# Performance work log

Measured on AMD Instinct MI355X. Metric: run time of the kernel, lower is better.

## Reference

```python
import jax, jax.numpy as jnp
import numpy as np

B, D, L, H = 256, 512, 64, 300


def setup_inputs() -> dict:
    key = jax.random.key(0)
    ks = jax.random.split(key, 16)
    s = 0.05  # weight init scale to keep activations sane through ReLU chains
    return {
        "x": jax.random.normal(ks[0], (B, D), jnp.float32),
        "eps": jax.random.normal(ks[1], (B, L), jnp.float32),
        "W": jax.random.normal(ks[2], (D, L), jnp.float32) * s,
        "enc1_w": jax.random.normal(ks[3], (H, D), jnp.float32) * s,
        "enc1_b": jax.random.normal(ks[4], (H,), jnp.float32) * s,
        "enc2_w": jax.random.normal(ks[5], (H, H), jnp.float32) * s,
        "enc2_b": jax.random.normal(ks[6], (H,), jnp.float32) * s,
        "zm_w": jax.random.normal(ks[7], (L, H), jnp.float32) * s,
        "zm_b": jax.random.normal(ks[8], (L,), jnp.float32) * s,
        "zv_w": jax.random.normal(ks[9], (L, H), jnp.float32) * s,
        "zv_b": jax.random.normal(ks[10], (L,), jnp.float32) * s,
        "gen1_w": jax.random.normal(ks[11], (H, L), jnp.float32) * s,
        "gen2_w": jax.random.normal(ks[12], (H, H), jnp.float32) * s,
        "gen2_b": jax.random.normal(ks[13], (H,), jnp.float32) * s,
        "head_w": jax.random.normal(ks[14], (D, H), jnp.float32) * s,
        "head_b": jax.random.normal(ks[15], (D,), jnp.float32) * s,
    }


def reference(x, eps, W, enc1_w, enc1_b, enc2_w, enc2_b, zm_w, zm_b,
              zv_w, zv_b, gen1_w, gen2_w, gen2_b, head_w, head_b):
    # encode: q_z = ReLU(Linear) -> ReLU(Linear)
    h = jax.nn.relu(x @ enc1_w.T + enc1_b)
    h = jax.nn.relu(h @ enc2_w.T + enc2_b)
    z_mean = h @ zm_w.T + zm_b          # [B, L]
    z_log_var = h @ zv_w.T + zv_b       # [B, L]
    # reparameterize (eps passed in for determinism)
    z = z_mean + eps * jnp.exp(0.5 * z_log_var)
    # decode: per-column masked z through shared generator + per-column head,
    # vectorized over the column axis D (mask = W rows)
    masked = z[:, None, :] * W[None, :, :]                       # [B, D, L]
    g1 = jax.nn.relu(jnp.einsum('bdl,hl->bdh', masked, gen1_w))  # [B, D, H]
    g2 = jax.nn.relu(jnp.einsum('bdh,gh->bdg', g1, gen2_w) + gen2_b)
    x_mean = jnp.einsum('bdh,dh->bd', g2, head_w) + head_b       # [B, D]
    return (x_mean, z, z_mean, z_log_var)
```

## Files before the change

kernel.cpp:

```cpp
#include <hip/hip_runtime.h>

typedef unsigned short u16;
typedef unsigned int u32;

typedef __bf16 bf16x8 __attribute__((ext_vector_type(8)));
typedef float f32x4 __attribute__((ext_vector_type(4)));

union V16 { uint4 u; bf16x8 v; u16 s[8]; __bf16 h[8]; };
union F4  { float4 v; float f[4]; };

__device__ __forceinline__ float bf2f(u16 a) {
  union { u32 u; float f; } c; c.u = ((u32)a) << 16; return c.f;
}

#define Z_OFF   131072
#define ZM_OFF  147456
#define ZLV_OFF 163840

#define B1_OFF 0
#define B2_OFF 2560
#define E1_OFF 15360
#define E2_OFF 35840
#define ZMP_OFF 48640
#define ZVP_OFF 51200
#define FRAG_TOTAL 53760
#define WB4  53760
#define XB4  57856
#define H1_4 74240
#define H2_4 84480
#define PACK_THREADS (FRAG_TOTAL + 4096 + 16384)

__device__ __forceinline__ void pack_one(const float* __restrict__ src,
                                         int t, int s, int lane,
                                         int Nsrc, int Ksrc, int rowlen,
                                         uint4* __restrict__ dst) {
  const int n = t * 16 + (lane & 15);
  const int k0 = s * 32 + ((lane >> 4) << 3);
  V16 v;
#pragma unroll
  for (int j = 0; j < 8; ++j) {
    const int k = k0 + j;
    v.h[j] = (n < Nsrc && k < Ksrc) ? (__bf16)src[n * rowlen + k] : (__bf16)0.f;
  }
  *dst = v.u;
}

__device__ __forceinline__ void cvt8(const float* __restrict__ src, uint4* __restrict__ dst) {
  F4 a, b; a.v = *(const float4*)src; b.v = *(const float4*)(src + 4);
  V16 v;
#pragma unroll
  for (int j = 0; j < 4; ++j) { v.h[j] = (__bf16)a.f[j]; v.h[4 + j] = (__bf16)b.f[j]; }
  *dst = v.u;
}

__global__ __launch_bounds__(256) void pack_kernel(
    const float* __restrict__ g1w, const float* __restrict__ g2w,
    const float* __restrict__ e1w, const float* __restrict__ e2w,
    const float* __restrict__ zmw, const float* __restrict__ zvw,
    const float* __restrict__ W,   const float* __restrict__ x,
    uint4* __restrict__ ws4) {
  const int idx = blockIdx.x * 256 + threadIdx.x;
  if (idx >= PACK_THREADS) return;
  const int lane = idx & 63;
  if (idx < B2_OFF) {
    const int f = (idx - B1_OFF) >> 6;
    pack_one(g1w, f >> 1, f & 1, lane, 300, 64, 64, ws4 + idx);
  } else if (idx < E1_OFF) {
    const int f = (idx - B2_OFF) >> 6;
    pack_one(g2w, f / 10, f % 10, lane, 300, 300, 300, ws4 + idx);
  } else if (idx < E2_OFF) {
    const int f = (idx - E1_OFF) >> 6;
    pack_one(e1w, f >> 4, f & 15, lane, 300, 512, 512, ws4 + idx);
  } else if (idx < ZMP_OFF) {
    const int f = (idx - E2_OFF) >> 6;
    pack_one(e2w, f / 10, f % 10, lane, 300, 300, 300, ws4 + idx);
  } else if (idx < ZVP_OFF) {
    const int f = (idx - ZMP_OFF) >> 6;
    pack_one(zmw, f / 10, f % 10, lane, 64, 300, 300, ws4 + idx);
  } else if (idx < FRAG_TOTAL) {
    const int f = (idx - ZVP_OFF) >> 6;
    pack_one(zvw, f / 10, f % 10, lane, 64, 300, 300, ws4 + idx);
  } else if (idx < FRAG_TOTAL + 4096) {
    const int i = idx - FRAG_TOTAL;
    cvt8(W + i * 8, ws4 + WB4 + i);
  } else {
    const int i = idx - FRAG_TOTAL - 4096;
    cvt8(x + i * 8, ws4 + XB4 + i);
  }
}

__global__ __launch_bounds__(64) void enc1_kernel(
    const uint4* __restrict__ xb, const uint4* __restrict__ e1p,
    const float* __restrict__ e1b, u16* __restrict__ h1) {
  const int wg = blockIdx.x;
  const int rt = wg / 20, nt = wg % 20;
  const int lane = threadIdx.x, q = lane >> 4, c = lane & 15;
  f32x4 acc = {0.f, 0.f, 0.f, 0.f};
  const int arow = rt * 16 + c;
#pragma unroll
  for (int s = 0; s < 16; ++s) {
    V16 a, b;
    a.u = xb[arow * 64 + s * 4 + q];
    b.u = e1p[(nt * 16 + s) * 64 + lane];
    acc = __builtin_amdgcn_mfma_f32_16x16x32_bf16(a.v, b.v, acc, 0, 0, 0);
  }
  const int col = nt * 16 + c;
  const float bias = (col < 300) ? e1b[col] : 0.f;
#pragma unroll
  for (int i = 0; i < 4; ++i) {
    const int row = rt * 16 + 4 * q + i;
    V16 t; t.h[0] = (col < 300) ? (__bf16)fmaxf(acc[i] + bias, 0.f) : (__bf16)0.f;
    h1[row * 320 + col] = t.s[0];
  }
}

__global__ __launch_bounds__(64) void enc2_kernel(
    const uint4* __restrict__ h1, const uint4* __restrict__ e2p,
    const float* __restrict__ e2b, u16* __restrict__ h2) {
  const int wg = blockIdx.x;
  const int rt = wg / 20, nt = wg % 20;
  const int lane = threadIdx.x, q = lane >> 4, c = lane & 15;
  f32x4 acc = {0.f, 0.f, 0.f, 0.f};
  const int arow = rt * 16 + c;
#pragma unroll
  for (int s = 0; s < 10; ++s) {
    V16 a, b;
    a.u = h1[arow * 40 + s * 4 + q];
    b.u = e2p[(nt * 10 + s) * 64 + lane];
    acc = __builtin_amdgcn_mfma_f32_16x16x32_bf16(a.v, b.v, acc, 0, 0, 0);
  }
  const int col = nt * 16 + c;
  const float bias = (col < 300) ? e2b[col] : 0.f;
#pragma unroll
  for (int i = 0; i < 4; ++i) {
    const int row = rt * 16 + 4 * q + i;
    V16 t; t.h[0] = (col < 300) ? (__bf16)fmaxf(acc[i] + bias, 0.f) : (__bf16)0.f;
    h2[row * 320 + col] = t.s[0];
  }
}

__global__ __launch_bounds__(64) void ench_kernel(
    const uint4* __restrict__ h2, const float* __restrict__ eps,
    const uint4* __restrict__ zmp, const float* __restrict__ zmb,
    const uint4* __restrict__ zvp, const float* __restrict__ zvb,
    float* __restrict__ out) {
  const int wg = blockIdx.x;
  const int rt = wg >> 2, t = wg & 3;
  const int lane = threadIdx.x, q = lane >> 4, c = lane & 15;
  f32x4 am = {0.f, 0.f, 0.f, 0.f}, av = {0.f, 0.f, 0.f, 0.f};
  const int arow = rt * 16 + c;
#pragma unroll
  for (int s = 0; s < 10; ++s) {
    V16 a, bm, bv;
    a.u = h2[arow * 40 + s * 4 + q];
    bm.u = zmp[(t * 10 + s) * 64 + lane];
    bv.u = zvp[(t * 10 + s) * 64 + lane];
    am = __builtin_amdgcn_mfma_f32_16x16x32_bf16(a.v, bm.v, am, 0, 0, 0);
    av = __builtin_amdgcn_mfma_f32_16x16x32_bf16(a.v, bv.v, av, 0, 0, 0);
  }
  const int col = t * 16 + c;
  const float bm = zmb[col], bv = zvb[col];
#pragma unroll
  for (int i = 0; i < 4; ++i) {
    const int gi = (rt * 16 + 4 * q + i) * 64 + col;
    const float zm = am[i] + bm;
    const float zlv = av[i] + bv;
    out[ZM_OFF + gi] = zm;
    out[ZLV_OFF + gi] = zlv;
    out[Z_OFF + gi] = zm + eps[gi] * expf(0.5f * zlv);
  }
}

__global__ __launch_bounds__(320, 4) void dec_kernel(
    const float* __restrict__ z,
    const uint4* __restrict__ Wb,
    const uint4* __restrict__ b1p,
    const uint4* __restrict__ b2p,
    const float* __restrict__ g2b,
    const float* __restrict__ hw,
    const float* __restrict__ hb,
    float* __restrict__ xout) {
  __shared__ u16 g1s[32 * 328];
  float* xredf = (float*)g1s;

  const int wg = blockIdx.x;
  const int r0 = wg << 5;
  const int bi = wg >> 4;
  const int d0 = r0 & 511;
  const int tid = threadIdx.x;
  const int u = tid >> 6;
  const int lane = tid & 63;
  const int q = lane >> 4;
  const int c = lane & 15;

  const float* zrow = z + bi * 64;

  bf16x8 bz[4][2];
#pragma unroll
  for (int kf = 0; kf < 2; ++kf) {
    F4 z0, z1;
    z0.v = *(const float4*)(zrow + kf * 32 + q * 8);
    z1.v = *(const float4*)(zrow + kf * 32 + q * 8 + 4);
#pragma unroll
    for (int tt = 0; tt < 4; ++tt) {
      V16 r; r.u = b1p[((4 * u + tt) * 2 + kf) * 64 + lane];
      V16 m;
#pragma unroll
      for (int j = 0; j < 4; ++j) {
        m.h[j]     = (__bf16)(bf2f(r.s[j])     * z0.f[j]);
        m.h[4 + j] = (__bf16)(bf2f(r.s[4 + j]) * z1.f[j]);
      }
      bz[tt][kf] = m.v;
    }
  }
#pragma unroll
  for (int rt = 0; rt < 2; ++rt) {
    const int rowA = rt * 16 + c;
    V16 af0, af1;
    af0.u = Wb[(d0 + rowA) * 8 + q];
    af1.u = Wb[(d0 + rowA) * 8 + 4 + q];
    f32x4 acc[4];
#pragma unroll
    for (int tt = 0; tt < 4; ++tt) acc[tt] = {0.f, 0.f, 0.f, 0.f};
#pragma unroll
    for (int tt = 0; tt < 4; ++tt) {
      acc[tt] = __builtin_amdgcn_mfma_f32_16x16x32_bf16(af0.v, bz[tt][0], acc[tt], 0, 0, 0);
      acc[tt] = __builtin_amdgcn_mfma_f32_16x16x32_bf16(af1.v, bz[tt][1], acc[tt], 0, 0, 0);
    }
    const int rwb = rt * 16 + 4 * q;
#pragma unroll
    for (int tt = 0; tt < 4; ++tt) {
      const int colb = (4 * u + tt) * 16 + c;
#pragma unroll
      for (int i = 0; i < 4; ++i) {
        V16 t; t.h[0] = (__bf16)fmaxf(acc[tt][i], 0.f);
        g1s[(rwb + i) * 328 + colb] = t.s[0];
      }
    }
  }
  __syncthreads();

  f32x4 a3[4][2];
#pragma unroll
  for (int tt = 0; tt < 4; ++tt)
#pragma unroll
    for (int rt = 0; rt < 2; ++rt) a3[tt][rt] = {0.f, 0.f, 0.f, 0.f};
  for (int s = 0; s < 10; ++s) {
    V16 b[4];
#pragma unroll
    for (int tt = 0; tt < 4; ++tt) b[tt].u = b2p[((4 * u + tt) * 10 + s) * 64 + lane];
#pragma unroll
    for (int rt = 0; rt < 2; ++rt) {
      V16 a; a.u = *(const uint4*)&g1s[(rt * 16 + c) * 328 + s * 32 + q * 8];
#pragma unroll
      for (int tt = 0; tt < 4; ++tt)
        a3[tt][rt] = __builtin_amdgcn_mfma_f32_16x16x32_bf16(a.v, b[tt].v, a3[tt][rt], 0, 0, 0);
    }
  }
  float xacc[2][4];
#pragma unroll
  for (int rt = 0; rt < 2; ++rt)
#pragma unroll
    for (int i = 0; i < 4; ++i) xacc[rt][i] = 0.f;
#pragma unroll
  for (int tt = 0; tt < 4; ++tt) {
    const int col = (4 * u + tt) * 16 + c;
    const bool inb = (col < 300);
    const float bias = inb ? g2b[col] : 0.f;
#pragma unroll
    for (int rt = 0; rt < 2; ++rt)
#pragma unroll
      for (int i = 0; i < 4; ++i) {
        const float g2v = fmaxf(a3[tt][rt][i] + bias, 0.f);
        const float h = inb ? hw[(d0 + rt * 16 + 4 * q + i) * 300 + col] : 0.f;
        xacc[rt][i] += g2v * h;
      }
  }
#pragma unroll
  for (int rt = 0; rt < 2; ++rt)
#pragma unroll
    for (int i = 0; i < 4; ++i) {
      float t = xacc[rt][i];
      t += __shfl_xor(t, 1);
      t += __shfl_xor(t, 2);
      t += __shfl_xor(t, 4);
      t += __shfl_xor(t, 8);
      xacc[rt][i] = t;
    }
  __syncthreads();
  if (c < 4) {
#pragma unroll
    for (int rt = 0; rt < 2; ++rt) {
      float t = xacc[rt][0];
      t = (c == 1) ? xacc[rt][1] : t;
      t = (c == 2) ? xacc[rt][2] : t;
      t = (c == 3) ? xacc[rt][3] : t;
      xredf[u * 32 + rt * 16 + 4 * q + c] = t;
    }
  }
  __syncthreads();
  if (tid < 32) {
    float t = hb[d0 + tid];
#pragma unroll
    for (int uu = 0; uu < 5; ++uu) t += xredf[uu * 32 + tid];
    xout[r0 + tid] = t;
  }
}

extern "C" void kernel_launch(void* const* d_in, const int* in_sizes, int n_in,
                              void* d_out, int out_size, void* d_ws, size_t ws_size,
                              hipStream_t stream) {
  const float* x   = (const float*)d_in[0];
  const float* eps = (const float*)d_in[1];
  const float* W   = (const float*)d_in[2];
  const float* e1w = (const float*)d_in[3];
  const float* e1b = (const float*)d_in[4];
  const float* e2w = (const float*)d_in[5];
  const float* e2b = (const float*)d_in[6];
  const float* zmw = (const float*)d_in[7];
  const float* zmb = (const float*)d_in[8];
  const float* zvw = (const float*)d_in[9];
  const float* zvb = (const float*)d_in[10];
  const float* g1w = (const float*)d_in[11];
  const float* g2w = (const float*)d_in[12];
  const float* g2b = (const float*)d_in[13];
  const float* hw  = (const float*)d_in[14];
  const float* hb  = (const float*)d_in[15];
  float* out = (float*)d_out;
  uint4* ws4 = (uint4*)d_ws;

  pack_kernel<<<(PACK_THREADS + 255) / 256, 256, 0, stream>>>(
      g1w, g2w, e1w, e2w, zmw, zvw, W, x, ws4);
  enc1_kernel<<<320, 64, 0, stream>>>(ws4 + XB4, ws4 + E1_OFF, e1b, (u16*)(ws4 + H1_4));
  enc2_kernel<<<320, 64, 0, stream>>>(ws4 + H1_4, ws4 + E2_OFF, e2b, (u16*)(ws4 + H2_4));
  ench_kernel<<<64, 64, 0, stream>>>(ws4 + H2_4, eps,
                                     ws4 + ZMP_OFF, zmb, ws4 + ZVP_OFF, zvb, out);
  dec_kernel<<<4096, 320, 0, stream>>>(out + Z_OFF, ws4 + WB4,
                                       ws4 + B1_OFF, ws4 + B2_OFF,
                                       g2b, hw, hb, out);
}
```

Before: 163.7 us.

## Fuse weight packing and the encoder MLP into one prep kernel

Replaces the pack, enc1, enc2 and z-head kernels with a single prep kernel. 16 blocks each run the whole encoder for 16 rows, keeping h1/h2 in shared memory and converting encoder weights to bf16 fragments on the fly from fp32. The remaining blocks pack the decoder weights and W concurrently. This removes three launches and the global round trips for the intermediates, but the encoder now runs on only 16 blocks and every block redundantly reconverts the encoder weights.

```diff
diff --git a/kernel.cpp b/kernel.cpp
--- a/kernel.cpp
+++ b/kernel.cpp
@@ -19,16 +19,10 @@
 
 #define B1_OFF 0
 #define B2_OFF 2560
-#define E1_OFF 15360
-#define E2_OFF 35840
-#define ZMP_OFF 48640
-#define ZVP_OFF 51200
-#define FRAG_TOTAL 53760
-#define WB4  53760
-#define XB4  57856
-#define H1_4 74240
-#define H2_4 84480
-#define PACK_THREADS (FRAG_TOTAL + 4096 + 16384)
+#define WB4   15360
+#define PACK_TOTAL 19456
+#define NENC 16
+#define PACK_BLOCKS ((PACK_TOTAL + 319) / 320)
 
 __device__ __forceinline__ void pack_one(const float* __restrict__ src,
                                          int t, int s, int lane,
@@ -53,121 +47,145 @@
   *dst = v.u;
 }
 
-__global__ __launch_bounds__(256) void pack_kernel(
+__device__ __forceinline__ uint4 mkfrag(const float* __restrict__ w, int n, int k0,
+                                        int N, int K, int ld) {
+  V16 v;
+  if (n < N && k0 + 7 < K) {
+    F4 a, b;
+    a.v = *(const float4*)(w + n * ld + k0);
+    b.v = *(const float4*)(w + n * ld + k0 + 4);
+#pragma unroll
+    for (int j = 0; j < 4; ++j) { v.h[j] = (__bf16)a.f[j]; v.h[4 + j] = (__bf16)b.f[j]; }
+  } else if (n < N) {
+#pragma unroll
+    for (int j = 0; j < 8; ++j) {
+      const int k = k0 + j;
+      v.h[j] = (k < K) ? (__bf16)w[n * ld + k] : (__bf16)0.f;
+    }
+  } else {
+    v.u = make_uint4(0u, 0u, 0u, 0u);
+  }
+  return v.u;
+}
+
+__global__ __launch_bounds__(320) void prep_kernel(
+    const float* __restrict__ x,   const float* __restrict__ eps,
+    const float* __restrict__ e1w, const float* __restrict__ e1b,
+    const float* __restrict__ e2w, const float* __restrict__ e2b,
+    const float* __restrict__ zmw, const float* __restrict__ zmb,
+    const float* __restrict__ zvw, const float* __restrict__ zvb,
     const float* __restrict__ g1w, const float* __restrict__ g2w,
-    const float* __restrict__ e1w, const float* __restrict__ e2w,
-    const float* __restrict__ zmw, const float* __restrict__ zvw,
-    const float* __restrict__ W,   const float* __restrict__ x,
-    uint4* __restrict__ ws4) {
-  const int idx = blockIdx.x * 256 + threadIdx.x;
-  if (idx >= PACK_THREADS) return;
-  const int lane = idx & 63;
-  if (idx < B2_OFF) {
-    const int f = (idx - B1_OFF) >> 6;
-    pack_one(g1w, f >> 1, f & 1, lane, 300, 64, 64, ws4 + idx);
-  } else if (idx < E1_OFF) {
-    const int f = (idx - B2_OFF) >> 6;
-    pack_one(g2w, f / 10, f % 10, lane, 300, 300, 300, ws4 + idx);
-  } else if (idx < E2_OFF) {
-    const int f = (idx - E1_OFF) >> 6;
-    pack_one(e1w, f >> 4, f & 15, lane, 300, 512, 512, ws4 + idx);
-  } else if (idx < ZMP_OFF) {
-    const int f = (idx - E2_OFF) >> 6;
-    pack_one(e2w, f / 10, f % 10, lane, 300, 300, 300, ws4 + idx);
-  } else if (idx < ZVP_OFF) {
-    const int f = (idx - ZMP_OFF) >> 6;
-    pack_one(zmw, f / 10, f % 10, lane, 64, 300, 300, ws4 + idx);
-  } else if (idx < FRAG_TOTAL) {
-    const int f = (idx - ZVP_OFF) >> 6;
-    pack_one(zvw, f / 10, f % 10, lane, 64, 300, 300, ws4 + idx);
-  } else if (idx < FRAG_TOTAL + 4096) {
-    const int i = idx - FRAG_TOTAL;
-    cvt8(W + i * 8, ws4 + WB4 + i);
-  } else {
-    const int i = idx - FRAG_TOTAL - 4096;
-    cvt8(x + i * 8, ws4 + XB4 + i);
-  }
-}
-
-__global__ __launch_bounds__(64) void enc1_kernel(
-    const uint4* __restrict__ xb, const uint4* __restrict__ e1p,
-    const float* __restrict__ e1b, u16* __restrict__ h1) {
-  const int wg = blockIdx.x;
-  const int rt = wg / 20, nt = wg % 20;
-  const int lane = threadIdx.x, q = lane >> 4, c = lane & 15;
-  f32x4 acc = {0.f, 0.f, 0.f, 0.f};
-  const int arow = rt * 16 + c;
-#pragma unroll
-  for (int s = 0; s < 16; ++s) {
-    V16 a, b;
-    a.u = xb[arow * 64 + s * 4 + q];
-    b.u = e1p[(nt * 16 + s) * 64 + lane];
-    acc = __builtin_amdgcn_mfma_f32_16x16x32_bf16(a.v, b.v, acc, 0, 0, 0);
-  }
-  const int col = nt * 16 + c;
-  const float bias = (col < 300) ? e1b[col] : 0.f;
-#pragma unroll
-  for (int i = 0; i < 4; ++i) {
-    const int row = rt * 16 + 4 * q + i;
-    V16 t; t.h[0] = (col < 300) ? (__bf16)fmaxf(acc[i] + bias, 0.f) : (__bf16)0.f;
-    h1[row * 320 + col] = t.s[0];
-  }
-}
-
-__global__ __launch_bounds__(64) void enc2_kernel(
-    const uint4* __restrict__ h1, const uint4* __restrict__ e2p,
-    const float* __restrict__ e2b, u16* __restrict__ h2) {
-  const int wg = blockIdx.x;
-  const int rt = wg / 20, nt = wg % 20;
-  const int lane = threadIdx.x, q = lane >> 4, c = lane & 15;
-  f32x4 acc = {0.f, 0.f, 0.f, 0.f};
-  const int arow = rt * 16 + c;
-#pragma unroll
-  for (int s = 0; s < 10; ++s) {
-    V16 a, b;
-    a.u = h1[arow * 40 + s * 4 + q];
-    b.u = e2p[(nt * 10 + s) * 64 + lane];
-    acc = __builtin_amdgcn_mfma_f32_16x16x32_bf16(a.v, b.v, acc, 0, 0, 0);
-  }
-  const int col = nt * 16 + c;
-  const float bias = (col < 300) ? e2b[col] : 0.f;
-#pragma unroll
-  for (int i = 0; i < 4; ++i) {
-    const int row = rt * 16 + 4 * q + i;
-    V16 t; t.h[0] = (col < 300) ? (__bf16)fmaxf(acc[i] + bias, 0.f) : (__bf16)0.f;
-    h2[row * 320 + col] = t.s[0];
-  }
-}
-
-__global__ __launch_bounds__(64) void ench_kernel(
-    const uint4* __restrict__ h2, const float* __restrict__ eps,
-    const uint4* __restrict__ zmp, const float* __restrict__ zmb,
-    const uint4* __restrict__ zvp, const float* __restrict__ zvb,
-    float* __restrict__ out) {
-  const int wg = blockIdx.x;
-  const int rt = wg >> 2, t = wg & 3;
-  const int lane = threadIdx.x, q = lane >> 4, c = lane & 15;
-  f32x4 am = {0.f, 0.f, 0.f, 0.f}, av = {0.f, 0.f, 0.f, 0.f};
-  const int arow = rt * 16 + c;
-#pragma unroll
-  for (int s = 0; s < 10; ++s) {
-    V16 a, bm, bv;
-    a.u = h2[arow * 40 + s * 4 + q];
-    bm.u = zmp[(t * 10 + s) * 64 + lane];
-    bv.u = zvp[(t * 10 + s) * 64 + lane];
-    am = __builtin_amdgcn_mfma_f32_16x16x32_bf16(a.v, bm.v, am, 0, 0, 0);
-    av = __builtin_amdgcn_mfma_f32_16x16x32_bf16(a.v, bv.v, av, 0, 0, 0);
-  }
-  const int col = t * 16 + c;
-  const float bm = zmb[col], bv = zvb[col];
-#pragma unroll
-  for (int i = 0; i < 4; ++i) {
-    const int gi = (rt * 16 + 4 * q + i) * 64 + col;
-    const float zm = am[i] + bm;
-    const float zlv = av[i] + bv;
-    out[ZM_OFF + gi] = zm;
-    out[ZLV_OFF + gi] = zlv;
-    out[Z_OFF + gi] = zm + eps[gi] * expf(0.5f * zlv);
+    const float* __restrict__ W,
+    uint4* __restrict__ ws4, float* __restrict__ out) {
+  __shared__ uint4 xs[16 * 65];
+  __shared__ u16  h1s[16 * 328];
+  u16* h2s = (u16*)xs;
+
+  const int blk = blockIdx.x;
+  const int tid = threadIdx.x;
+
+  if (blk >= NENC) {
+    const int idx = (blk - NENC) * 320 + tid;
+    if (idx >= PACK_TOTAL) return;
+    const int lane = idx & 63;
+    if (idx < B2_OFF) {
+      const int f = idx >> 6;
+      pack_one(g1w, f >> 1, f & 1, lane, 300, 64, 64, ws4 + B1_OFF + idx);
+    } else if (idx < WB4) {
+      const int f = (idx - B2_OFF) >> 6;
+      pack_one(g2w, f / 10, f % 10, lane, 300, 300, 300, ws4 + idx);
+    } else {
+      const int i = idx - WB4;
+      cvt8(W + i * 8, ws4 + WB4 + i);
+    }
+    return;
+  }
+
+  const int u = tid >> 6;
+  const int lane = tid & 63;
+  const int q = lane >> 4, c = lane & 15;
+  const int r0 = blk * 16;
+
+  for (int i = tid; i < 1024; i += 320) {
+    const int row = i >> 6, kg = i & 63;
+    cvt8(x + (r0 + row) * 512 + kg * 8, &xs[row * 65 + kg]);
+  }
+  __syncthreads();
+
+  {
+    f32x4 acc[4];
+#pragma unroll
+    for (int tt = 0; tt < 4; ++tt) acc[tt] = {0.f, 0.f, 0.f, 0.f};
+#pragma unroll 4
+    for (int s = 0; s < 16; ++s) {
+      V16 a; a.u = xs[c * 65 + s * 4 + q];
+#pragma unroll
+      for (int tt = 0; tt < 4; ++tt) {
+        V16 b; b.u = mkfrag(e1w, (4 * u + tt) * 16 + c, s * 32 + q * 8, 300, 512, 512);
+        acc[tt] = __builtin_amdgcn_mfma_f32_16x16x32_bf16(a.v, b.v, acc[tt], 0, 0, 0);
+      }
+    }
+#pragma unroll
+    for (int tt = 0; tt < 4; ++tt) {
+      const int col = (4 * u + tt) * 16 + c;
+      const float bias = (col < 300) ? e1b[col] : 0.f;
+#pragma unroll
+      for (int i = 0; i < 4; ++i) {
+        V16 t; t.h[0] = (col < 300) ? (__bf16)fmaxf(acc[tt][i] + bias, 0.f) : (__bf16)0.f;
+        h1s[(4 * q + i) * 328 + col] = t.s[0];
+      }
+    }
+  }
+  __syncthreads();
+
+  {
+    f32x4 acc[4];
+#pragma unroll
+    for (int tt = 0; tt < 4; ++tt) acc[tt] = {0.f, 0.f, 0.f, 0.f};
+#pragma unroll 2
+    for (int s = 0; s < 10; ++s) {
+      V16 a; a.u = *(const uint4*)&h1s[c * 328 + s * 32 + q * 8];
+#pragma unroll
+      for (int tt = 0; tt < 4; ++tt) {
+        V16 b; b.u = mkfrag(e2w, (4 * u + tt) * 16 + c, s * 32 + q * 8, 300, 300, 300);
+        acc[tt] = __builtin_amdgcn_mfma_f32_16x16x32_bf16(a.v, b.v, acc[tt], 0, 0, 0);
+      }
+    }
+#pragma unroll
+    for (int tt = 0; tt < 4; ++tt) {
+      const int col = (4 * u + tt) * 16 + c;
+      const float bias = (col < 300) ? e2b[col] : 0.f;
+#pragma unroll
+      for (int i = 0; i < 4; ++i) {
+        V16 t; t.h[0] = (col < 300) ? (__bf16)fmaxf(acc[tt][i] + bias, 0.f) : (__bf16)0.f;
+        h2s[(4 * q + i) * 328 + col] = t.s[0];
+      }
+    }
+  }
+  __syncthreads();
+
+  if (u < 4) {
+    f32x4 am = {0.f, 0.f, 0.f, 0.f}, av = {0.f, 0.f, 0.f, 0.f};
+#pragma unroll 2
+    for (int s = 0; s < 10; ++s) {
+      V16 a; a.u = *(const uint4*)&h2s[c * 328 + s * 32 + q * 8];
+      V16 bm, bv;
+      bm.u = mkfrag(zmw, u * 16 + c, s * 32 + q * 8, 64, 300, 300);
+      bv.u = mkfrag(zvw, u * 16 + c, s * 32 + q * 8, 64, 300, 300);
+      am = __builtin_amdgcn_mfma_f32_16x16x32_bf16(a.v, bm.v, am, 0, 0, 0);
+      av = __builtin_amdgcn_mfma_f32_16x16x32_bf16(a.v, bv.v, av, 0, 0, 0);
+    }
+    const int col = u * 16 + c;
+    const float bm = zmb[col], bv = zvb[col];
+#pragma unroll
+    for (int i = 0; i < 4; ++i) {
+      const int gi = (r0 + 4 * q + i) * 64 + col;
+      const float zm = am[i] + bm;
+      const float zlv = av[i] + bv;
+      out[ZM_OFF + gi] = zm;
+      out[ZLV_OFF + gi] = zlv;
+      out[Z_OFF + gi] = zm + eps[gi] * expf(0.5f * zlv);
+    }
   }
 }
 
@@ -329,12 +347,8 @@
   float* out = (float*)d_out;
   uint4* ws4 = (uint4*)d_ws;
 
-  pack_kernel<<<(PACK_THREADS + 255) / 256, 256, 0, stream>>>(
-      g1w, g2w, e1w, e2w, zmw, zvw, W, x, ws4);
-  enc1_kernel<<<320, 64, 0, stream>>>(ws4 + XB4, ws4 + E1_OFF, e1b, (u16*)(ws4 + H1_4));
-  enc2_kernel<<<320, 64, 0, stream>>>(ws4 + H1_4, ws4 + E2_OFF, e2b, (u16*)(ws4 + H2_4));
-  ench_kernel<<<64, 64, 0, stream>>>(ws4 + H2_4, eps,
-                                     ws4 + ZMP_OFF, zmb, ws4 + ZVP_OFF, zvb, out);
+  prep_kernel<<<NENC + PACK_BLOCKS, 320, 0, stream>>>(
+      x, eps, e1w, e1b, e2w, e2b, zmw, zmb, zvw, zvb, g1w, g2w, W, ws4, out);
   dec_kernel<<<4096, 320, 0, stream>>>(out + Z_OFF, ws4 + WB4,
                                        ws4 + B1_OFF, ws4 + B2_OFF,
                                        g2b, hw, hb, out);
```

Result: slower. 202.5 us (+23.7%).
